# Performance work log

Measured on AMD Instinct MI355X. Metric: run time of the kernel, lower is better.

Reference implementation:

```python
import jax, jax.numpy as jnp
import numpy as np


def setup_inputs() -> dict:
    key = jax.random.key(0)
    k1, k2, k3 = jax.random.split(key, 3)
    B, S, IN, OUT = 2, 4096, 4096, 11008
    # int8 activations and weights, matching torch.randint(-127, 127, ...)
    x = jax.random.randint(k1, (B, S, IN), -127, 127, dtype=jnp.int8)
    weight = jax.random.randint(k2, (OUT, IN), -127, 127, dtype=jnp.int8)
    bias = jax.random.normal(k3, (1, OUT), dtype=jnp.float32)
    alpha = jnp.array(1e-3, dtype=jnp.float32)  # input_scale * weight_scale
    return {"x": x, "weight": weight, "bias": bias, "alpha": alpha}


def reference(x, weight, bias, alpha):
    # y = SiLU(alpha * (x_i8 @ W_i8^T) + beta * bias), beta = 1.0, output fp32
    x_shape = x.shape
    x2d = x.reshape(-1, x_shape[-1])  # [N, in]
    acc = jnp.matmul(x2d.astype(jnp.int32), weight.T.astype(jnp.int32))  # [N, out] int32
    y = alpha * acc.astype(jnp.float32) + bias  # fused dequant + bias epilogue
    y = y * jax.nn.sigmoid(y)  # SiLU
    return y.reshape(*x_shape[:-1], -1)
```

## Files before the change

### kernel.cpp

```cpp
#include <hip/hip_runtime.h>
#include <stdint.h>

#define BM 256
#define BN 256
#define BKB 128

typedef __attribute__((ext_vector_type(4)))  int i32x4;
typedef __attribute__((ext_vector_type(16))) int i32x16;

__device__ __forceinline__ void async16(const void* g, void* l) {
    __builtin_amdgcn_global_load_lds(
        (const __attribute__((address_space(1))) unsigned int*)g,
        (__attribute__((address_space(3))) unsigned int*)l,
        16 , 0 , 0 );
}

__global__ void pack_both(const int4* __restrict__ sx, int* __restrict__ dx, int nx4,
                          const int4* __restrict__ sw, int* __restrict__ dw, int nw4) {
    int idx    = blockIdx.x * blockDim.x + threadIdx.x;
    int stride = gridDim.x * blockDim.x;
    for (int i = idx; i < nx4; i += stride) {
        int4 a = sx[i];
        dx[i] = (a.x & 0xFF) | ((a.y & 0xFF) << 8) | ((a.z & 0xFF) << 16) | (a.w << 24);
    }
    for (int i = idx; i < nw4; i += stride) {
        int4 a = sw[i];
        dw[i] = (a.x & 0xFF) | ((a.y & 0xFF) << 8) | ((a.z & 0xFF) << 16) | (a.w << 24);
    }
}

__global__ __launch_bounds__(512, 2) void w8a8_silu_kernel(
    const int8_t* __restrict__ x, const int8_t* __restrict__ w,
    const float* __restrict__ bias, const float* __restrict__ alpha_p,
    float* __restrict__ out, int M, int N, int K, int nbn)
{
    __shared__ int8_t lds_a[2][BM * BKB];
    __shared__ int8_t lds_b[2][BN * BKB];

    const int tid  = threadIdx.x;
    const int lane = tid & 63;
    const int wave = tid >> 6;

    int bid = blockIdx.x;
    const int nwg = gridDim.x;
    if ((nwg & 7) == 0) bid = (bid & 7) * (nwg >> 3) + (bid >> 3);
    const int bm = bid / nbn;
    const int bn = bid - bm * nbn;

    const int srow  = tid >> 3;
    const int skoff = (((tid & 7) ^ ((tid >> 3) & 7)) << 4);
    const int8_t* gA = x + ((size_t)bm * BM + srow) * K + skoff;
    const int8_t* gB = w + ((size_t)bn * BN + srow) * K + skoff;
    const int ldst = tid * 16;

    const int wr  = (wave >> 2) * 128;
    const int wc  = (wave & 3) * 64;
    const int l31 = lane & 31;
    const int q2  = lane >> 5;
    const int xr  = l31 & 7;

    i32x16 acc[4][2] = {};

    const int NT = K / BKB;

#define STAGE_A(T, BUF) { const size_t kk = (size_t)(T) * BKB;                       \
    _Pragma("unroll") for (int j = 0; j < 4; ++j)                                     \
        async16(gA + (size_t)(j * 64) * K + kk, &lds_a[BUF][j * 8192 + ldst]); }
#define STAGE_B(T, BUF) { const size_t kk = (size_t)(T) * BKB;                       \
    _Pragma("unroll") for (int j = 0; j < 4; ++j)                                     \
        async16(gB + (size_t)(j * 64) * K + kk, &lds_b[BUF][j * 8192 + ldst]); }

#define READF(S, KS) {                                                                \
    const int ck_ = (((KS) * 2 + q2) ^ xr) << 4;                                      \
    _Pragma("unroll") for (int f = 0; f < 4; ++f)                                     \
        af[S][f] = *(const i32x4*)(la + ((wr + f * 32 + l31) << 7) + ck_);            \
    _Pragma("unroll") for (int f = 0; f < 2; ++f)                                     \
        bf[S][f] = *(const i32x4*)(lb + ((wc + f * 32 + l31) << 7) + ck_); }

    STAGE_A(0, 0);
    STAGE_B(0, 0);
    asm volatile("s_waitcnt vmcnt(0)" ::: "memory");
    __builtin_amdgcn_s_barrier();

    for (int t = 0; t < NT; ++t) {
        const int cb = t & 1;
        const int8_t* la = lds_a[cb];
        const int8_t* lb = lds_b[cb];

        i32x4 af[2][4], bf[2][2];
        READF(0, 0);
        if (t + 1 < NT) {
            STAGE_A(t + 1, cb ^ 1);
            STAGE_B(t + 1, cb ^ 1);
        }

#pragma unroll
        for (int ks = 0; ks < 4; ++ks) {
            const int cu = ks & 1;
            if (ks < 3) { const int nx = cu ^ 1; READF(nx, ks + 1); }
            __builtin_amdgcn_s_setprio(1);
#pragma unroll
            for (int mf = 0; mf < 4; ++mf)
#pragma unroll
                for (int nf = 0; nf < 2; ++nf)
                    acc[mf][nf] = __builtin_amdgcn_mfma_i32_32x32x32_i8(
                        af[cu][mf], bf[cu][nf], acc[mf][nf], 0, 0, 0);
            __builtin_amdgcn_s_setprio(0);
        }

        asm volatile("s_waitcnt vmcnt(0)" ::: "memory");
        __builtin_amdgcn_s_barrier();
        __builtin_amdgcn_sched_barrier(0);
    }

    const float alpha = *alpha_p;
    const int rowb = bm * BM + wr;
    const int colb = bn * BN + wc;
#pragma unroll
    for (int nf = 0; nf < 2; ++nf) {
        const int col = colb + nf * 32 + l31;
        const float bv = bias[col];
#pragma unroll
        for (int mf = 0; mf < 4; ++mf) {
#pragma unroll
            for (int r = 0; r < 16; ++r) {
                const int row = rowb + mf * 32 + (r & 3) + ((r >> 2) << 3) + (q2 << 2);
                float y = fmaf(alpha, (float)acc[mf][nf][r], bv);
                out[(size_t)row * N + col] = y / (1.0f + __expf(-y));
            }
        }
    }
}

extern "C" void kernel_launch(void* const* d_in, const int* in_sizes, int n_in,
                              void* d_out, int out_size, void* d_ws, size_t ws_size,
                              hipStream_t stream) {
    const int*   x32   = (const int*)d_in[0];
    const int*   w32   = (const int*)d_in[1];
    const float* bias  = (const float*)d_in[2];
    const float* alpha = (const float*)d_in[3];
    float*       out   = (float*)d_out;

    const int N = in_sizes[2];
    const int K = in_sizes[1] / N;
    const int M = in_sizes[0] / K;

    int8_t* x8 = (int8_t*)d_ws;
    int8_t* w8 = x8 + (size_t)M * K;

    const int nx4 = (int)(((size_t)M * K) / 4);
    const int nw4 = (int)(((size_t)N * K) / 4);
    pack_both<<<2048, 256, 0, stream>>>((const int4*)x32, (int*)x8, nx4,
                                        (const int4*)w32, (int*)w8, nw4);

    const int nbm = M / BM, nbn = N / BN;
    w8a8_silu_kernel<<<nbm * nbn, 512, 0, stream>>>(x8, w8, bias, alpha, out, M, N, K, nbn);
}
```

Before: 949.1 us.

## Halve K tile and use a four-stage async LDS pipeline with one barrier

Shrinks the K tile from 128 to 64 bytes and turns the double-buffered LDS scheme into a four-buffer ring that keeps three tiles of global-to-LDS loads in flight. Waits use graded vmcnt counts, and there is a single barrier at the top of each iteration. The LDS swizzle is rewritten as a rotation for the narrower 64-byte rows. The aim is to hide global load latency better and cut the full drain stall that previously ended every iteration. The cost is more iterations with less MFMA work each. There is also a possible visibility hazard, because a wave may read LDS filled by other waves' async loads without a barrier after its own wait.

```diff
diff --git a/kernel.cpp b/kernel.cpp
--- a/kernel.cpp
+++ b/kernel.cpp
@@ -3,7 +3,7 @@
 
 #define BM 256
 #define BN 256
-#define BKB 128
+#define BKB 64
 
 typedef __attribute__((ext_vector_type(4)))  int i32x4;
 typedef __attribute__((ext_vector_type(16))) int i32x16;
@@ -34,8 +34,8 @@
     const float* __restrict__ bias, const float* __restrict__ alpha_p,
     float* __restrict__ out, int M, int N, int K, int nbn)
 {
-    __shared__ int8_t lds_a[2][BM * BKB];
-    __shared__ int8_t lds_b[2][BN * BKB];
+    __shared__ int8_t lds_a[4][BM * BKB];
+    __shared__ int8_t lds_b[4][BN * BKB];
 
     const int tid  = threadIdx.x;
     const int lane = tid & 63;
@@ -47,8 +47,8 @@
     const int bm = bid / nbn;
     const int bn = bid - bm * nbn;
 
-    const int srow  = tid >> 3;
-    const int skoff = (((tid & 7) ^ ((tid >> 3) & 7)) << 4);
+    const int srow  = tid >> 2;
+    const int skoff = ((((tid & 3) - ((tid >> 3) & 3)) & 3) << 4);
     const int8_t* gA = x + ((size_t)bm * BM + srow) * K + skoff;
     const int8_t* gB = w + ((size_t)bn * BN + srow) * K + skoff;
     const int ldst = tid * 16;
@@ -57,60 +57,61 @@
     const int wc  = (wave & 3) * 64;
     const int l31 = lane & 31;
     const int q2  = lane >> 5;
-    const int xr  = l31 & 7;
+    const int cq  = (l31 >> 1) & 3;
 
     i32x16 acc[4][2] = {};
 
     const int NT = K / BKB;
 
-#define STAGE_A(T, BUF) { const size_t kk = (size_t)(T) * BKB;                       \
-    _Pragma("unroll") for (int j = 0; j < 4; ++j)                                     \
-        async16(gA + (size_t)(j * 64) * K + kk, &lds_a[BUF][j * 8192 + ldst]); }
-#define STAGE_B(T, BUF) { const size_t kk = (size_t)(T) * BKB;                       \
-    _Pragma("unroll") for (int j = 0; j < 4; ++j)                                     \
-        async16(gB + (size_t)(j * 64) * K + kk, &lds_b[BUF][j * 8192 + ldst]); }
+#define STAGE(T, BUF) { const size_t kk = (size_t)(T) * BKB;                          \
+    async16(gA + kk,                    &lds_a[BUF][ldst]);                           \
+    async16(gA + (size_t)128 * K + kk,  &lds_a[BUF][8192 + ldst]);                    \
+    async16(gB + kk,                    &lds_b[BUF][ldst]);                           \
+    async16(gB + (size_t)128 * K + kk,  &lds_b[BUF][8192 + ldst]); }
 
 #define READF(S, KS) {                                                                \
-    const int ck_ = (((KS) * 2 + q2) ^ xr) << 4;                                      \
+    const int ck_ = ((((KS) * 2 + q2) + cq) & 3) << 4;                                \
     _Pragma("unroll") for (int f = 0; f < 4; ++f)                                     \
-        af[S][f] = *(const i32x4*)(la + ((wr + f * 32 + l31) << 7) + ck_);            \
+        af[S][f] = *(const i32x4*)(la + ((wr + f * 32 + l31) << 6) + ck_);            \
     _Pragma("unroll") for (int f = 0; f < 2; ++f)                                     \
-        bf[S][f] = *(const i32x4*)(lb + ((wc + f * 32 + l31) << 7) + ck_); }
+        bf[S][f] = *(const i32x4*)(lb + ((wc + f * 32 + l31) << 6) + ck_); }
 
-    STAGE_A(0, 0);
-    STAGE_B(0, 0);
-    asm volatile("s_waitcnt vmcnt(0)" ::: "memory");
-    __builtin_amdgcn_s_barrier();
+    STAGE(0, 0);
+    STAGE(1, 1);
+    STAGE(2, 2);
 
     for (int t = 0; t < NT; ++t) {
-        const int cb = t & 1;
+        const int cb = t & 3;
+
+        __builtin_amdgcn_s_barrier();
+        __builtin_amdgcn_sched_barrier(0);
+
+        if (t + 3 < NT) STAGE(t + 3, (t + 3) & 3);
+
+        const int rem = NT - 1 - t;
+        if      (rem >= 3) asm volatile("s_waitcnt vmcnt(12)" ::: "memory");
+        else if (rem == 2) asm volatile("s_waitcnt vmcnt(8)"  ::: "memory");
+        else if (rem == 1) asm volatile("s_waitcnt vmcnt(4)"  ::: "memory");
+        else               asm volatile("s_waitcnt vmcnt(0)"  ::: "memory");
+
         const int8_t* la = lds_a[cb];
         const int8_t* lb = lds_b[cb];
 
         i32x4 af[2][4], bf[2][2];
         READF(0, 0);
-        if (t + 1 < NT) {
-            STAGE_A(t + 1, cb ^ 1);
-            STAGE_B(t + 1, cb ^ 1);
-        }
+        READF(1, 1);
 
 #pragma unroll
-        for (int ks = 0; ks < 4; ++ks) {
-            const int cu = ks & 1;
-            if (ks < 3) { const int nx = cu ^ 1; READF(nx, ks + 1); }
+        for (int ks = 0; ks < 2; ++ks) {
             __builtin_amdgcn_s_setprio(1);
 #pragma unroll
             for (int mf = 0; mf < 4; ++mf)
 #pragma unroll
                 for (int nf = 0; nf < 2; ++nf)
                     acc[mf][nf] = __builtin_amdgcn_mfma_i32_32x32x32_i8(
-                        af[cu][mf], bf[cu][nf], acc[mf][nf], 0, 0, 0);
+                        af[ks][mf], bf[ks][nf], acc[mf][nf], 0, 0, 0);
             __builtin_amdgcn_s_setprio(0);
         }
-
-        asm volatile("s_waitcnt vmcnt(0)" ::: "memory");
-        __builtin_amdgcn_s_barrier();
-        __builtin_amdgcn_sched_barrier(0);
     }
 
     const float alpha = *alpha_p;
```

Measured after the change: 1.064 ms. 12.1% more time.
